# Optimization experiments

Hardware: AMD Instinct MI355X
Metric: run time of the kernel (lower is better)

## Reference

```python
import jax, jax.numpy as jnp
import numpy as np

BETA = 0.2  # encoder_fit_vq_factor
K = 4096    # codebook_size
D = 256     # codeword_size
B, T = 8, 2048


def setup_inputs() -> dict:
    key = jax.random.key(0)
    k1, k2 = jax.random.split(key)
    x = jax.random.normal(k1, (B, T, D), dtype=jnp.float32)
    # torch init: uniform(-1/n^2, 1/n^2) with n=1 -> uniform(-1, 1)
    embedding = jax.random.uniform(k2, (K, D), dtype=jnp.float32, minval=-1.0, maxval=1.0)
    return {"x": x, "embedding": embedding}


def reference(x, embedding):
    dist = (
        jnp.sum(x * x, axis=2, keepdims=True)
        + jnp.sum(embedding * embedding, axis=1)
        - 2.0 * jnp.einsum("btd,kd->btk", x, embedding)
    )
    indexes = jnp.argmin(dist, axis=2)  # [B, T]
    # one_hot @ embedding is just a gather (same math, no [B,T,K] one-hot)
    values = jnp.take(embedding, indexes, axis=0)  # [B, T, D]
    loss1 = jnp.mean((jax.lax.stop_gradient(x) - values) ** 2)
    loss2 = jnp.mean((x - jax.lax.stop_gradient(values)) ** 2)
    out = x + jax.lax.stop_gradient(values - x)  # straight-through estimator
    return out, indexes, loss1 + BETA * loss2
```

## Files before the change

### kernel.cpp

```cpp
#include <hip/hip_runtime.h>
#include <hip/hip_bf16.h>

#define N_ROWS 16384
#define K_CODES 4096
#define D_DIM 256

typedef short short8 __attribute__((ext_vector_type(8)));
typedef float floatx4 __attribute__((ext_vector_type(4)));

__device__ inline void gload_lds16(const void* g, void* l) {
    __builtin_amdgcn_global_load_lds(
        (const __attribute__((address_space(1))) void*)g,
        (__attribute__((address_space(3))) void*)l, 16, 0, 0);
}

__global__ __launch_bounds__(256) void vq_prep(const float* __restrict__ x,
                                               const float* __restrict__ e,
                                               float* __restrict__ en,
                                               float* __restrict__ xx) {
    int tid  = threadIdx.x;
    int w    = blockIdx.x * 4 + (tid >> 6);
    int lane = tid & 63;
    const float* src;
    float* dst;
    if (w < K_CODES) { src = e + (size_t)w * D_DIM;             dst = en + w; }
    else             { src = x + (size_t)(w - K_CODES) * D_DIM; dst = xx + (w - K_CODES); }
    float4 v = reinterpret_cast<const float4*>(src)[lane];
    float s = v.x * v.x + v.y * v.y + v.z * v.z + v.w * v.w;
#pragma unroll
    for (int m = 32; m; m >>= 1) s += __shfl_xor(s, m, 64);
    if (lane == 0) *dst = s;
}

__global__ __launch_bounds__(256) void vq_pack(const float* __restrict__ x,
                                               const float* __restrict__ e,
                                               uint4* __restrict__ X,
                                               uint4* __restrict__ E) {
    int tid  = threadIdx.x;
    int w    = blockIdx.x * 4 + (tid >> 6);
    int lane = tid & 63;
    int ri = lane >> 3, part = (lane >> 2) & 1, ps = lane & 3;

    const float* src;
    uint4* img;
    int rg, ch;
    if (w < 16384) { rg = w >> 3;            ch = w & 7; src = x; img = X; }
    else           { int v = w - 16384; rg = v >> 3; ch = v & 7; src = e; img = E; }

    int row = rg * 8 + ri;
    int b   = row >> 7, rl = row & 127;
    int d0  = ch * 32 + ((ps ^ (rl & 3)) * 8);

    const float* p = src + (size_t)row * D_DIM + d0;
    float4 v0 = reinterpret_cast<const float4*>(p)[0];
    float4 v1 = reinterpret_cast<const float4*>(p)[1];
    float f[8] = {v0.x, v0.y, v0.z, v0.w, v1.x, v1.y, v1.z, v1.w};
    unsigned int bts[8];
#pragma unroll
    for (int i = 0; i < 8; ++i) {
        unsigned int u = __float_as_uint(f[i]);
        if (part == 0) bts[i] = u >> 16;
        else {
            float lo = f[i] - __uint_as_float(u & 0xFFFF0000u);
            bts[i] = __float_as_uint(lo) >> 16;
        }
    }
    img[(size_t)b * 8192 + ch * 1024 + (rg & 15) * 64 + lane] =
        make_uint4(bts[0] | (bts[1] << 16), bts[2] | (bts[3] << 16),
                   bts[4] | (bts[5] << 16), bts[6] | (bts[7] << 16));
}

__global__ __launch_bounds__(256) void vq_argmin(const uint4* __restrict__ X,
                                                 const uint4* __restrict__ E,
                                                 const float* __restrict__ en,
                                                 const float* __restrict__ xx,
                                                 unsigned long long* __restrict__ top2) {
    __shared__ __align__(16) unsigned short sm[2048 * 8];

    int tid  = threadIdx.x;
    int cbk  = blockIdx.x & 31;
    int rb   = blockIdx.x >> 5;
    int r0   = rb * 128, c0 = cbk * 128;
    int lane = tid & 63;
    int wave = tid >> 6;
    int wm   = wave >> 1, wn = wave & 1;
    int l15  = lane & 15, lq = lane >> 4;

    floatx4 acc[4][4];
#pragma unroll
    for (int mt = 0; mt < 4; ++mt)
#pragma unroll
        for (int nt = 0; nt < 4; ++nt) acc[mt][nt] = (floatx4)0.f;

    const uint4* Ag = X + (size_t)rb  * 8192;
    const uint4* Bg = E + (size_t)cbk * 8192;

    const short8* Av = reinterpret_cast<const short8*>(sm);
    int uaq = (l15 & 7) * 8 + (lq ^ (l15 & 3));
    int A0  = (wm * 8 + (l15 >> 3)) * 64 + uaq;
    int B0  = 1024 + (wn * 8 + (l15 >> 3)) * 64 + uaq;

    for (int ch = 0; ch < 8; ++ch) {
        __syncthreads();
#pragma unroll
        for (int i = 0; i < 4; ++i) {
            int q = i * 256 + tid;
            gload_lds16(Ag + ch * 1024 + q, (char*)sm + (i * 256 + wave * 64) * 16);
            gload_lds16(Bg + ch * 1024 + q, (char*)sm + ((1024 + i * 256) + wave * 64) * 16);
        }
        __syncthreads();

        short8 ah[4], al[4];
#pragma unroll
        for (int t = 0; t < 4; ++t) {
            ah[t] = Av[A0 + t * 128];
            al[t] = Av[A0 + t * 128 + 4];
        }
#pragma unroll
        for (int nt = 0; nt < 4; ++nt) {
            short8 bh = Av[B0 + nt * 128];
            short8 bl = Av[B0 + nt * 128 + 4];
#pragma unroll
            for (int mt = 0; mt < 4; ++mt) {
                acc[mt][nt] = __builtin_amdgcn_mfma_f32_16x16x32_bf16(ah[mt], bh, acc[mt][nt], 0, 0, 0);
                acc[mt][nt] = __builtin_amdgcn_mfma_f32_16x16x32_bf16(ah[mt], bl, acc[mt][nt], 0, 0, 0);
                acc[mt][nt] = __builtin_amdgcn_mfma_f32_16x16x32_bf16(al[mt], bh, acc[mt][nt], 0, 0, 0);
            }
        }
    }

    float xv[4][4], ev[4];
#pragma unroll
    for (int mt = 0; mt < 4; ++mt)
#pragma unroll
        for (int r = 0; r < 4; ++r)
            xv[mt][r] = xx[r0 + wm * 64 + mt * 16 + lq * 4 + r];
#pragma unroll
    for (int nt = 0; nt < 4; ++nt) ev[nt] = en[c0 + wn * 64 + nt * 16 + l15];

    __syncthreads();
    unsigned long long* cand = (unsigned long long*)sm;

#pragma unroll
    for (int mt = 0; mt < 4; ++mt) {
#pragma unroll
        for (int r = 0; r < 4; ++r) {
            unsigned int b0 = 0xFFFFFFFFu, b1 = 0xFFFFFFFFu;
#pragma unroll
            for (int nt = 0; nt < 4; ++nt) {
                float dist = (xv[mt][r] + ev[nt]) - 2.0f * acc[mt][nt][r];
                unsigned int u = __float_as_uint(dist);
                u ^= (u & 0x80000000u) ? 0xFFFFFFFFu : 0x80000000u;
                unsigned int key = (u & 0xFFFFF000u) |
                                   (unsigned)(c0 + wn * 64 + nt * 16 + l15);
                if (key < b0) { b1 = b0; b0 = key; }
                else if (key < b1) b1 = key;
            }
            int row_local = wm * 64 + mt * 16 + lq * 4 + r;
            cand[(row_local * 2 + wn) * 16 + l15] =
                ((unsigned long long)b0 << 32) | b1;
        }
    }
    __syncthreads();

    {
        unsigned int B0 = 0xFFFFFFFFu, B1 = 0xFFFFFFFFu;
        const unsigned long long* cb = cand + tid * 16;
#pragma unroll
        for (int j = 0; j < 8; ++j) {
            int o = ((j + tid) & 7) * 2;
            unsigned long long p0 = cb[o], p1 = cb[o + 1];
            unsigned int o0 = (unsigned int)(p0 >> 32), o1 = (unsigned int)p0;
            unsigned int mx = B0 > o0 ? B0 : o0;
            B0 = B0 < o0 ? B0 : o0;
            unsigned int mn = B1 < o1 ? B1 : o1;
            B1 = mx < mn ? mx : mn;
            o0 = (unsigned int)(p1 >> 32); o1 = (unsigned int)p1;
            mx = B0 > o0 ? B0 : o0;
            B0 = B0 < o0 ? B0 : o0;
            mn = B1 < o1 ? B1 : o1;
            B1 = mx < mn ? mx : mn;
        }
        top2[(size_t)(r0 + (tid >> 1)) * 64 + cbk * 2 + (tid & 1)] =
            ((unsigned long long)B0 << 32) | B1;
    }
}

__global__ __launch_bounds__(256) void vq_merge(const float* __restrict__ x,
                                                const float* __restrict__ e,
                                                const float* __restrict__ en,
                                                const float* __restrict__ xx,
                                                const unsigned long long* __restrict__ top2,
                                                float* __restrict__ out,
                                                double* __restrict__ partials) {
    int tid  = threadIdx.x;
    int lane = tid & 63;
    int wave = tid >> 6;
    int row  = blockIdx.x * 4 + wave;

    unsigned long long c = top2[(size_t)row * 64 + lane];
    unsigned int k0 = (unsigned int)(c >> 32);
    unsigned int k1 = (unsigned int)c;
    unsigned int k2 = 0xFFFFFFFFu, k3 = 0xFFFFFFFFu;
#pragma unroll
    for (int m = 1; m <= 32; m <<= 1) {
        unsigned int o0 = __shfl_xor(k0, m, 64);
        unsigned int o1 = __shfl_xor(k1, m, 64);
        unsigned int o2 = __shfl_xor(k2, m, 64);
        unsigned int o3 = __shfl_xor(k3, m, 64);
        unsigned int t0 = min(k0, o0), s0 = max(k0, o0);
        unsigned int t1 = min(k1, o1), s1 = max(k1, o1);
        unsigned int t2 = min(k2, o2);
        unsigned int t3 = min(k3, o3);
        k0 = t0;
        k1 = min(s0, t1);
        unsigned int u = max(s0, t1);
        k2 = min(u, t2);
        k3 = min(max(u, t2), min(s1, t3));
    }
    int i0 = k0 & 0xFFF, i1 = k1 & 0xFFF, i2 = k2 & 0xFFF, i3 = k3 & 0xFFF;

    float4 xv = reinterpret_cast<const float4*>(x)[(size_t)row * 64 + lane];
    float4 e0 = reinterpret_cast<const float4*>(e)[(size_t)i0 * 64 + lane];
    float4 e1 = reinterpret_cast<const float4*>(e)[(size_t)i1 * 64 + lane];
    float4 e2 = reinterpret_cast<const float4*>(e)[(size_t)i2 * 64 + lane];
    float4 e3 = reinterpret_cast<const float4*>(e)[(size_t)i3 * 64 + lane];
    double p0 = (double)xv.x * e0.x + (double)xv.y * e0.y + (double)xv.z * e0.z + (double)xv.w * e0.w;
    double p1 = (double)xv.x * e1.x + (double)xv.y * e1.y + (double)xv.z * e1.z + (double)xv.w * e1.w;
    double p2 = (double)xv.x * e2.x + (double)xv.y * e2.y + (double)xv.z * e2.z + (double)xv.w * e2.w;
    double p3 = (double)xv.x * e3.x + (double)xv.y * e3.y + (double)xv.z * e3.z + (double)xv.w * e3.w;
#pragma unroll
    for (int m = 32; m; m >>= 1) {
        p0 += __shfl_xor(p0, m, 64);
        p1 += __shfl_xor(p1, m, 64);
        p2 += __shfl_xor(p2, m, 64);
        p3 += __shfl_xor(p3, m, 64);
    }
    double xr = (double)xx[row];
    double d0 = (xr + (double)en[i0]) - 2.0 * p0;
    double d1 = (xr + (double)en[i1]) - 2.0 * p1;
    double d2 = (xr + (double)en[i2]) - 2.0 * p2;
    double d3 = (xr + (double)en[i3]) - 2.0 * p3;

    double bd = d0; int bi = i0; float4 v = e0;
    if (d1 < bd || (d1 == bd && i1 < bi)) { bd = d1; bi = i1; v = e1; }
    if (d2 < bd || (d2 == bd && i2 < bi)) { bd = d2; bi = i2; v = e2; }
    if (d3 < bd || (d3 == bd && i3 < bi)) { bd = d3; bi = i3; v = e3; }

    float4 o;
    o.x = xv.x + (v.x - xv.x);
    o.y = xv.y + (v.y - xv.y);
    o.z = xv.z + (v.z - xv.z);
    o.w = xv.w + (v.w - xv.w);
    reinterpret_cast<float4*>(out)[(size_t)row * 64 + lane] = o;
    if (lane == 0) out[(size_t)N_ROWS * D_DIM + row] = (float)bi;

    float sx = xv.x - v.x, sy = xv.y - v.y, sz = xv.z - v.z, sw = xv.w - v.w;
    float ls = sx * sx + sy * sy + sz * sz + sw * sw;
#pragma unroll
    for (int m = 32; m; m >>= 1) ls += __shfl_xor(ls, m, 64);
    __shared__ float lred[4];
    if (lane == 0) lred[wave] = ls;
    __syncthreads();
    if (tid == 0)
        partials[blockIdx.x] = (double)lred[0] + (double)lred[1]
                             + (double)lred[2] + (double)lred[3];
}

__global__ __launch_bounds__(256) void vq_final(const double* __restrict__ partials,
                                                float* __restrict__ out) {
    int tid = threadIdx.x;
    double s = 0.0;
#pragma unroll
    for (int i = 0; i < 16; ++i) s += partials[tid + i * 256];
#pragma unroll
    for (int m = 32; m; m >>= 1) s += __shfl_xor(s, m, 64);
    __shared__ double dred[4];
    if ((tid & 63) == 0) dred[tid >> 6] = s;
    __syncthreads();
    if (tid == 0) {
        double tot = dred[0] + dred[1] + dred[2] + dred[3];
        float L = (float)(tot / (double)((size_t)N_ROWS * D_DIM));
        out[(size_t)N_ROWS * D_DIM + N_ROWS] = L + 0.2f * L;
    }
}

extern "C" void kernel_launch(void* const* d_in, const int* in_sizes, int n_in,
                              void* d_out, int out_size, void* d_ws, size_t ws_size,
                              hipStream_t stream) {
    const float* x = (const float*)d_in[0];
    const float* e = (const float*)d_in[1];
    float* out = (float*)d_out;
    char* ws = (char*)d_ws;
    double* partials = (double*)ws;
    float* en = (float*)(ws + 32768);
    float* xx = (float*)(ws + 49152);
    unsigned long long* top2 = (unsigned long long*)(ws + 114688);
    uint4* Ximg = (uint4*)(ws + 8503296);
    uint4* Eimg = (uint4*)(ws + 25280512);

    vq_prep<<<5120, 256, 0, stream>>>(x, e, en, xx);
    vq_pack<<<5120, 256, 0, stream>>>(x, e, Ximg, Eimg);
    vq_argmin<<<4096, 256, 0, stream>>>(Ximg, Eimg, en, xx, top2);
    vq_merge<<<4096, 256, 0, stream>>>(x, e, en, xx, top2, out, partials);
    vq_final<<<1, 256, 0, stream>>>(partials, out);
}
```

Before: 197.8 us.

## Drop row-norm term from distances and relayout packed hi/lo bf16 tiles

The ||x||^2 term is constant per row, so it is removed from the argmin distance and from the merge recheck. That eliminates the x-norm pass in the prep kernel, which now processes only codebook rows. The merge kernel recomputes ||e||^2 in double from the gathered codewords instead of reading the precomputed norms. The packed image layout also changes so hi and lo bf16 parts sit in separate 512-entry halves per chunk, with matching LDS index math in the argmin kernel. Dropping the norm changes float rounding in the 20-bit truncated keys, but the exact top-4 recheck should still select the correct index.

```diff
diff --git a/kernel.cpp b/kernel.cpp
--- a/kernel.cpp
+++ b/kernel.cpp
@@ -14,22 +14,16 @@
         (__attribute__((address_space(3))) void*)l, 16, 0, 0);
 }
 
-__global__ __launch_bounds__(256) void vq_prep(const float* __restrict__ x,
-                                               const float* __restrict__ e,
-                                               float* __restrict__ en,
-                                               float* __restrict__ xx) {
+__global__ __launch_bounds__(256) void vq_prep(const float* __restrict__ e,
+                                               float* __restrict__ en) {
     int tid  = threadIdx.x;
     int w    = blockIdx.x * 4 + (tid >> 6);
     int lane = tid & 63;
-    const float* src;
-    float* dst;
-    if (w < K_CODES) { src = e + (size_t)w * D_DIM;             dst = en + w; }
-    else             { src = x + (size_t)(w - K_CODES) * D_DIM; dst = xx + (w - K_CODES); }
-    float4 v = reinterpret_cast<const float4*>(src)[lane];
+    float4 v = reinterpret_cast<const float4*>(e + (size_t)w * D_DIM)[lane];
     float s = v.x * v.x + v.y * v.y + v.z * v.z + v.w * v.w;
 #pragma unroll
     for (int m = 32; m; m >>= 1) s += __shfl_xor(s, m, 64);
-    if (lane == 0) *dst = s;
+    if (lane == 0) en[w] = s;
 }
 
 __global__ __launch_bounds__(256) void vq_pack(const float* __restrict__ x,
@@ -39,17 +33,20 @@
     int tid  = threadIdx.x;
     int w    = blockIdx.x * 4 + (tid >> 6);
     int lane = tid & 63;
-    int ri = lane >> 3, part = (lane >> 2) & 1, ps = lane & 3;
+    int ri = lane >> 2, ps = lane & 3;
 
     const float* src;
     uint4* img;
-    int rg, ch;
-    if (w < 16384) { rg = w >> 3;            ch = w & 7; src = x; img = X; }
-    else           { int v = w - 16384; rg = v >> 3; ch = v & 7; src = e; img = E; }
-
-    int row = rg * 8 + ri;
-    int b   = row >> 7, rl = row & 127;
-    int d0  = ch * 32 + ((ps ^ (rl & 3)) * 8);
+    int rg, part, ch, b;
+    if (w < 16384) { rg = w & 7; part = (w >> 3) & 1; ch = (w >> 4) & 7; b = w >> 7;
+                     src = x; img = X; }
+    else           { int v = w - 16384;
+                     rg = v & 7; part = (v >> 3) & 1; ch = (v >> 4) & 7; b = v >> 7;
+                     src = e; img = E; }
+
+    int rl  = rg * 16 + ri;
+    int row = b * 128 + rl;
+    int d0  = ch * 32 + ((ps ^ (ri & 3)) * 8);
 
     const float* p = src + (size_t)row * D_DIM + d0;
     float4 v0 = reinterpret_cast<const float4*>(p)[0];
@@ -65,7 +62,7 @@
             bts[i] = __float_as_uint(lo) >> 16;
         }
     }
-    img[(size_t)b * 8192 + ch * 1024 + (rg & 15) * 64 + lane] =
+    img[(size_t)b * 8192 + ch * 1024 + part * 512 + rg * 64 + lane] =
         make_uint4(bts[0] | (bts[1] << 16), bts[2] | (bts[3] << 16),
                    bts[4] | (bts[5] << 16), bts[6] | (bts[7] << 16));
 }
@@ -73,7 +70,6 @@
 __global__ __launch_bounds__(256) void vq_argmin(const uint4* __restrict__ X,
                                                  const uint4* __restrict__ E,
                                                  const float* __restrict__ en,
-                                                 const float* __restrict__ xx,
                                                  unsigned long long* __restrict__ top2) {
     __shared__ __align__(16) unsigned short sm[2048 * 8];
 
@@ -96,9 +92,9 @@
     const uint4* Bg = E + (size_t)cbk * 8192;
 
     const short8* Av = reinterpret_cast<const short8*>(sm);
-    int uaq = (l15 & 7) * 8 + (lq ^ (l15 & 3));
-    int A0  = (wm * 8 + (l15 >> 3)) * 64 + uaq;
-    int B0  = 1024 + (wn * 8 + (l15 >> 3)) * 64 + uaq;
+    int sw = lq ^ (l15 & 3);
+    int ua = (wm * 64 + l15) * 4 + sw;
+    int ub = (wn * 64 + l15) * 4 + sw;
 
     for (int ch = 0; ch < 8; ++ch) {
         __syncthreads();
@@ -113,13 +109,13 @@
         short8 ah[4], al[4];
 #pragma unroll
         for (int t = 0; t < 4; ++t) {
-            ah[t] = Av[A0 + t * 128];
-            al[t] = Av[A0 + t * 128 + 4];
+            ah[t] = Av[ua + t * 64];
+            al[t] = Av[512 + ua + t * 64];
         }
 #pragma unroll
         for (int nt = 0; nt < 4; ++nt) {
-            short8 bh = Av[B0 + nt * 128];
-            short8 bl = Av[B0 + nt * 128 + 4];
+            short8 bh = Av[1024 + ub + nt * 64];
+            short8 bl = Av[1536 + ub + nt * 64];
 #pragma unroll
             for (int mt = 0; mt < 4; ++mt) {
                 acc[mt][nt] = __builtin_amdgcn_mfma_f32_16x16x32_bf16(ah[mt], bh, acc[mt][nt], 0, 0, 0);
@@ -129,12 +125,7 @@
         }
     }
 
-    float xv[4][4], ev[4];
-#pragma unroll
-    for (int mt = 0; mt < 4; ++mt)
-#pragma unroll
-        for (int r = 0; r < 4; ++r)
-            xv[mt][r] = xx[r0 + wm * 64 + mt * 16 + lq * 4 + r];
+    float ev[4];
 #pragma unroll
     for (int nt = 0; nt < 4; ++nt) ev[nt] = en[c0 + wn * 64 + nt * 16 + l15];
 
@@ -148,7 +139,7 @@
             unsigned int b0 = 0xFFFFFFFFu, b1 = 0xFFFFFFFFu;
 #pragma unroll
             for (int nt = 0; nt < 4; ++nt) {
-                float dist = (xv[mt][r] + ev[nt]) - 2.0f * acc[mt][nt][r];
+                float dist = ev[nt] - 2.0f * acc[mt][nt][r];
                 unsigned int u = __float_as_uint(dist);
                 u ^= (u & 0x80000000u) ? 0xFFFFFFFFu : 0x80000000u;
                 unsigned int key = (u & 0xFFFFF000u) |
@@ -188,8 +179,6 @@
 
 __global__ __launch_bounds__(256) void vq_merge(const float* __restrict__ x,
                                                 const float* __restrict__ e,
-                                                const float* __restrict__ en,
-                                                const float* __restrict__ xx,
                                                 const unsigned long long* __restrict__ top2,
                                                 float* __restrict__ out,
                                                 double* __restrict__ partials) {
@@ -229,18 +218,25 @@
     double p1 = (double)xv.x * e1.x + (double)xv.y * e1.y + (double)xv.z * e1.z + (double)xv.w * e1.w;
     double p2 = (double)xv.x * e2.x + (double)xv.y * e2.y + (double)xv.z * e2.z + (double)xv.w * e2.w;
     double p3 = (double)xv.x * e3.x + (double)xv.y * e3.y + (double)xv.z * e3.z + (double)xv.w * e3.w;
+    double q0 = (double)e0.x * e0.x + (double)e0.y * e0.y + (double)e0.z * e0.z + (double)e0.w * e0.w;
+    double q1 = (double)e1.x * e1.x + (double)e1.y * e1.y + (double)e1.z * e1.z + (double)e1.w * e1.w;
+    double q2 = (double)e2.x * e2.x + (double)e2.y * e2.y + (double)e2.z * e2.z + (double)e2.w * e2.w;
+    double q3 = (double)e3.x * e3.x + (double)e3.y * e3.y + (double)e3.z * e3.z + (double)e3.w * e3.w;
 #pragma unroll
     for (int m = 32; m; m >>= 1) {
         p0 += __shfl_xor(p0, m, 64);
         p1 += __shfl_xor(p1, m, 64);
         p2 += __shfl_xor(p2, m, 64);
         p3 += __shfl_xor(p3, m, 64);
-    }
-    double xr = (double)xx[row];
-    double d0 = (xr + (double)en[i0]) - 2.0 * p0;
-    double d1 = (xr + (double)en[i1]) - 2.0 * p1;
-    double d2 = (xr + (double)en[i2]) - 2.0 * p2;
-    double d3 = (xr + (double)en[i3]) - 2.0 * p3;
+        q0 += __shfl_xor(q0, m, 64);
+        q1 += __shfl_xor(q1, m, 64);
+        q2 += __shfl_xor(q2, m, 64);
+        q3 += __shfl_xor(q3, m, 64);
+    }
+    double d0 = q0 - 2.0 * p0;
+    double d1 = q1 - 2.0 * p1;
+    double d2 = q2 - 2.0 * p2;
+    double d3 = q3 - 2.0 * p3;
 
     double bd = d0; int bi = i0; float4 v = e0;
     if (d1 < bd || (d1 == bd && i1 < bi)) { bd = d1; bi = i1; v = e1; }
@@ -294,14 +290,13 @@
     char* ws = (char*)d_ws;
     double* partials = (double*)ws;
     float* en = (float*)(ws + 32768);
-    float* xx = (float*)(ws + 49152);
     unsigned long long* top2 = (unsigned long long*)(ws + 114688);
     uint4* Ximg = (uint4*)(ws + 8503296);
     uint4* Eimg = (uint4*)(ws + 25280512);
 
-    vq_prep<<<5120, 256, 0, stream>>>(x, e, en, xx);
+    vq_prep<<<1024, 256, 0, stream>>>(e, en);
     vq_pack<<<5120, 256, 0, stream>>>(x, e, Ximg, Eimg);
-    vq_argmin<<<4096, 256, 0, stream>>>(Ximg, Eimg, en, xx, top2);
-    vq_merge<<<4096, 256, 0, stream>>>(x, e, en, xx, top2, out, partials);
+    vq_argmin<<<4096, 256, 0, stream>>>(Ximg, Eimg, en, top2);
+    vq_merge<<<4096, 256, 0, stream>>>(x, e, top2, out, partials);
     vq_final<<<1, 256, 0, stream>>>(partials, out);
 }
```

Result: slower. 202.1 us (+2.2%).

## Fuse norm prep into pack kernel and split hi/lo planes in image layout

Applied to the files above, without the earlier changes.

Merges the squared-norm kernel into the bf16 packing kernel as extra blocks, removing one launch. Also changes the packed image layout so the hi and lo bf16 parts sit in separate 512-entry halves per chunk, with each row's 4 quads contiguous. The argmin LDS addressing is updated to match. This is meant to cut launch overhead and give cleaner LDS and global access patterns, but it risks changing the bank-conflict behaviour of the LDS reads.

```diff
diff --git a/kernel.cpp b/kernel.cpp
--- a/kernel.cpp
+++ b/kernel.cpp
@@ -14,60 +14,62 @@
         (__attribute__((address_space(3))) void*)l, 16, 0, 0);
 }
 
-__global__ __launch_bounds__(256) void vq_prep(const float* __restrict__ x,
+__global__ __launch_bounds__(256) void vq_pack(const float* __restrict__ x,
                                                const float* __restrict__ e,
+                                               uint4* __restrict__ X,
+                                               uint4* __restrict__ E,
                                                float* __restrict__ en,
                                                float* __restrict__ xx) {
     int tid  = threadIdx.x;
-    int w    = blockIdx.x * 4 + (tid >> 6);
     int lane = tid & 63;
-    const float* src;
-    float* dst;
-    if (w < K_CODES) { src = e + (size_t)w * D_DIM;             dst = en + w; }
-    else             { src = x + (size_t)(w - K_CODES) * D_DIM; dst = xx + (w - K_CODES); }
-    float4 v = reinterpret_cast<const float4*>(src)[lane];
-    float s = v.x * v.x + v.y * v.y + v.z * v.z + v.w * v.w;
-#pragma unroll
-    for (int m = 32; m; m >>= 1) s += __shfl_xor(s, m, 64);
-    if (lane == 0) *dst = s;
-}
-
-__global__ __launch_bounds__(256) void vq_pack(const float* __restrict__ x,
-                                               const float* __restrict__ e,
-                                               uint4* __restrict__ X,
-                                               uint4* __restrict__ E) {
-    int tid  = threadIdx.x;
-    int w    = blockIdx.x * 4 + (tid >> 6);
-    int lane = tid & 63;
-    int ri = lane >> 3, part = (lane >> 2) & 1, ps = lane & 3;
-
-    const float* src;
-    uint4* img;
-    int rg, ch;
-    if (w < 16384) { rg = w >> 3;            ch = w & 7; src = x; img = X; }
-    else           { int v = w - 16384; rg = v >> 3; ch = v & 7; src = e; img = E; }
-
-    int row = rg * 8 + ri;
-    int b   = row >> 7, rl = row & 127;
-    int d0  = ch * 32 + ((ps ^ (rl & 3)) * 8);
-
-    const float* p = src + (size_t)row * D_DIM + d0;
-    float4 v0 = reinterpret_cast<const float4*>(p)[0];
-    float4 v1 = reinterpret_cast<const float4*>(p)[1];
-    float f[8] = {v0.x, v0.y, v0.z, v0.w, v1.x, v1.y, v1.z, v1.w};
-    unsigned int bts[8];
-#pragma unroll
-    for (int i = 0; i < 8; ++i) {
-        unsigned int u = __float_as_uint(f[i]);
-        if (part == 0) bts[i] = u >> 16;
-        else {
-            float lo = f[i] - __uint_as_float(u & 0xFFFF0000u);
-            bts[i] = __float_as_uint(lo) >> 16;
-        }
-    }
-    img[(size_t)b * 8192 + ch * 1024 + (rg & 15) * 64 + lane] =
-        make_uint4(bts[0] | (bts[1] << 16), bts[2] | (bts[3] << 16),
-                   bts[4] | (bts[5] << 16), bts[6] | (bts[7] << 16));
+    if (blockIdx.x < 5120) {
+        int w  = blockIdx.x * 4 + (tid >> 6);
+        int ri = lane >> 2, ps = lane & 3;
+        const float* src;
+        uint4* img;
+        int rg, part, ch, b;
+        if (w < 16384) { rg = w & 7; part = (w >> 3) & 1; ch = (w >> 4) & 7; b = w >> 7;
+                         src = x; img = X; }
+        else           { int v = w - 16384;
+                         rg = v & 7; part = (v >> 3) & 1; ch = (v >> 4) & 7; b = v >> 7;
+                         src = e; img = E; }
+        int rl  = rg * 16 + ri;
+        int row = b * 128 + rl;
+        int d0  = ch * 32 + ((ps ^ (ri & 3)) * 8);
+
+        const float* p = src + (size_t)row * D_DIM + d0;
+        float4 v0 = reinterpret_cast<const float4*>(p)[0];
+        float4 v1 = reinterpret_cast<const float4*>(p)[1];
+        float f[8] = {v0.x, v0.y, v0.z, v0.w, v1.x, v1.y, v1.z, v1.w};
+        unsigned int bts[8];
+#pragma unroll
+        for (int i = 0; i < 8; ++i) {
+            unsigned int u = __float_as_uint(f[i]);
+            if (part == 0) bts[i] = u >> 16;
+            else {
+                float lo = f[i] - __uint_as_float(u & 0xFFFF0000u);
+                bts[i] = __float_as_uint(lo) >> 16;
+            }
+        }
+        img[(size_t)b * 8192 + ch * 1024 + part * 512 + rg * 64 + lane] =
+            make_uint4(bts[0] | (bts[1] << 16), bts[2] | (bts[3] << 16),
+                       bts[4] | (bts[5] << 16), bts[6] | (bts[7] << 16));
+    } else {
+        int w = (blockIdx.x - 5120) * 4 + (tid >> 6);
+#pragma unroll
+        for (int k = 0; k < 4; ++k) {
+            int r = w * 4 + k;
+            const float* src;
+            float* dst;
+            if (r < K_CODES) { src = e + (size_t)r * D_DIM;             dst = en + r; }
+            else             { src = x + (size_t)(r - K_CODES) * D_DIM; dst = xx + (r - K_CODES); }
+            float4 v = reinterpret_cast<const float4*>(src)[lane];
+            float s = v.x * v.x + v.y * v.y + v.z * v.z + v.w * v.w;
+#pragma unroll
+            for (int m = 32; m; m >>= 1) s += __shfl_xor(s, m, 64);
+            if (lane == 0) *dst = s;
+        }
+    }
 }
 
 __global__ __launch_bounds__(256) void vq_argmin(const uint4* __restrict__ X,
@@ -96,9 +98,9 @@
     const uint4* Bg = E + (size_t)cbk * 8192;
 
     const short8* Av = reinterpret_cast<const short8*>(sm);
-    int uaq = (l15 & 7) * 8 + (lq ^ (l15 & 3));
-    int A0  = (wm * 8 + (l15 >> 3)) * 64 + uaq;
-    int B0  = 1024 + (wn * 8 + (l15 >> 3)) * 64 + uaq;
+    int sw = lq ^ (l15 & 3);
+    int ua = (wm * 64 + l15) * 4 + sw;
+    int ub = (wn * 64 + l15) * 4 + sw;
 
     for (int ch = 0; ch < 8; ++ch) {
         __syncthreads();
@@ -113,13 +115,13 @@
         short8 ah[4], al[4];
 #pragma unroll
         for (int t = 0; t < 4; ++t) {
-            ah[t] = Av[A0 + t * 128];
-            al[t] = Av[A0 + t * 128 + 4];
+            ah[t] = Av[ua + t * 64];
+            al[t] = Av[512 + ua + t * 64];
         }
 #pragma unroll
         for (int nt = 0; nt < 4; ++nt) {
-            short8 bh = Av[B0 + nt * 128];
-            short8 bl = Av[B0 + nt * 128 + 4];
+            short8 bh = Av[1024 + ub + nt * 64];
+            short8 bl = Av[1536 + ub + nt * 64];
 #pragma unroll
             for (int mt = 0; mt < 4; ++mt) {
                 acc[mt][nt] = __builtin_amdgcn_mfma_f32_16x16x32_bf16(ah[mt], bh, acc[mt][nt], 0, 0, 0);
@@ -299,8 +301,7 @@
     uint4* Ximg = (uint4*)(ws + 8503296);
     uint4* Eimg = (uint4*)(ws + 25280512);
 
-    vq_prep<<<5120, 256, 0, stream>>>(x, e, en, xx);
-    vq_pack<<<5120, 256, 0, stream>>>(x, e, Ximg, Eimg);
+    vq_pack<<<6400, 256, 0, stream>>>(x, e, Ximg, Eimg, en, xx);
     vq_argmin<<<4096, 256, 0, stream>>>(Ximg, Eimg, en, xx, top2);
     vq_merge<<<4096, 256, 0, stream>>>(x, e, en, xx, top2, out, partials);
     vq_final<<<1, 256, 0, stream>>>(partials, out);
```

Result: no change. 196.3 us (-0.8%).
